# Kernel tuning notes

Hardware: AMD Instinct MI355X
Metric: run time of the kernel (lower is better)

## Reference

```python
import jax, jax.numpy as jnp
import numpy as np


def _rotate_half(x):
    x1, x2 = jnp.split(x, 2, axis=-1)
    return jnp.concatenate((-x2, x1), axis=-1)


def setup_inputs() -> dict:
    key = jax.random.key(0)
    ks = jax.random.split(key, 8)
    B, T, C, H = 2, 2048, 1024, 16
    Dh = C // H
    x = jax.random.normal(ks[0], (B, T, C), dtype=jnp.float32)
    # RoPE tables (T, head_dim)
    inv_freq = 1.0 / (10000.0 ** (np.arange(0, Dh, 2, dtype=np.float32) / Dh))
    pos = np.arange(T, dtype=np.float32)
    freqs = np.einsum('t,f->tf', pos, inv_freq)
    emb = np.concatenate([freqs, freqs], axis=-1)
    cos = jnp.asarray(np.cos(emb), dtype=jnp.float32)
    sin = jnp.asarray(np.sin(emb), dtype=jnp.float32)
    # causal mask: 1 where attending allowed, 0 elsewhere
    mask = jnp.tril(jnp.ones((T, T), dtype=jnp.int32))
    s = 0.02
    Wq = jax.random.normal(ks[1], (C, C), dtype=jnp.float32) * s
    Wk = jax.random.normal(ks[2], (C, C), dtype=jnp.float32) * s
    Wv = jax.random.normal(ks[3], (C, C), dtype=jnp.float32) * s
    Wo = jax.random.normal(ks[4], (C, C), dtype=jnp.float32) * s
    return {"x": x, "cos": cos, "sin": sin, "mask": mask, "n_heads": H,
            "Wq": Wq, "Wk": Wk, "Wv": Wv, "Wo": Wo}


def reference(x, cos, sin, mask, n_heads, Wq, Wk, Wv, Wo):
    B, T, C = x.shape
    H = n_heads
    Dh = C // H
    scale = Dh ** (-0.5)
    # projections (torch Linear: x @ W.T), reshape to (B, H, T, Dh)
    def proj(W):
        return (x @ W.T).reshape(B, T, H, Dh).transpose(0, 2, 1, 3)
    q, k, v = proj(Wq), proj(Wk), proj(Wv)
    # RoPE: cos/sin broadcast as (1, 1, T, Dh)
    c = cos[None, None]
    s = sin[None, None]
    q = q * c + _rotate_half(q) * s
    k = k * c + _rotate_half(k) * s
    att = jnp.einsum('bhtd,bhsd->bhts', q, k) * scale
    att = jnp.where(mask == 0, -jnp.inf, att)
    att = jax.nn.softmax(att, axis=-1)
    out = jnp.einsum('bhts,bhsd->bhtd', att, v)
    out = out.transpose(0, 2, 1, 3).reshape(B, T, C)
    return out @ Wo.T
```

## Files before the change

kernel.cpp:

```cpp
#include <hip/hip_runtime.h>
#include <stdint.h>

#define B_   2
#define T_   2048
#define C_   1024
#define H_   16
#define BT   4096
#define KDIM 1024

typedef unsigned short u16;
typedef __attribute__((ext_vector_type(8))) __bf16 bf16v8;
typedef __attribute__((ext_vector_type(4))) float f32x4;
typedef __attribute__((ext_vector_type(16))) float f32x16;
typedef __attribute__((ext_vector_type(4))) unsigned int u32x4;
typedef __attribute__((ext_vector_type(2))) unsigned int u32x2;

#define MFMA16(a, b, c) __builtin_amdgcn_mfma_f32_16x16x32_bf16((a), (b), (c), 0, 0, 0)
#define MFMA32(a, b, c) __builtin_amdgcn_mfma_f32_32x32x16_bf16((a), (b), (c), 0, 0, 0)

#define BARRIER() do { asm volatile("" ::: "memory"); \
                       __builtin_amdgcn_s_barrier();  \
                       asm volatile("" ::: "memory"); } while (0)

__device__ __forceinline__ u16 f2bf(float f) {
  __bf16 h = (__bf16)f;
  union { __bf16 h; u16 u; } v; v.h = h;
  return v.u;
}

__device__ __forceinline__ void xhalf(uint32_t a, uint32_t b,
                                      uint32_t& lo, uint32_t& hi) {
#if defined(__has_builtin) && __has_builtin(__builtin_amdgcn_permlane32_swap)
  u32x2 r = __builtin_amdgcn_permlane32_swap(a, b, false, false);
  lo = r.x; hi = r.y;
#else
  const bool upper = (threadIdx.x & 32) != 0;
  lo = upper ? __shfl_xor(b, 32) : a;
  hi = upper ? b : __shfl_xor(a, 32);
#endif
}

__device__ __forceinline__ void gload16(const void* g, void* l) {
  __builtin_amdgcn_global_load_lds((__attribute__((address_space(1))) void*)g,
                                   (__attribute__((address_space(3))) void*)l,
                                   16, 0, 0);
}

__global__ __launch_bounds__(256) void cvt_f32_bf16(const float* __restrict__ in,
                                                    u16* __restrict__ out, int n) {
  int i = (blockIdx.x * 256 + threadIdx.x) * 4;
  if (i + 3 < n) {
    float4 v = *(const float4*)(in + i);
    ushort4 o;
    o.x = f2bf(v.x); o.y = f2bf(v.y); o.z = f2bf(v.z); o.w = f2bf(v.w);
    *(ushort4*)(out + i) = o;
  }
}

__global__ __launch_bounds__(256) void cvt_weights(
    const float* __restrict__ wq, const float* __restrict__ wk,
    const float* __restrict__ wv, const float* __restrict__ wo,
    u16* __restrict__ qkv_dst, u16* __restrict__ o_dst) {
  const int bid = blockIdx.x;
  const int sel = bid >> 10;
  const float* src = (sel == 0) ? wq : (sel == 1) ? wk : (sel == 2) ? wv : wo;
  u16* dst = (sel < 3) ? (qkv_dst + sel * 1048576) : o_dst;
  const int i = ((bid & 1023) * 256 + threadIdx.x) * 4;
  float4 v = *(const float4*)(src + i);
  ushort4 o;
  o.x = f2bf(v.x); o.y = f2bf(v.y); o.z = f2bf(v.z); o.w = f2bf(v.w);
  *(ushort4*)(dst + i) = o;
}

template<int EPI, int NN>
__global__ __launch_bounds__(256, 2) void gemm128(
    const u16* __restrict__ A, const u16* __restrict__ Bm,
    float* __restrict__ Cf,
    u16* __restrict__ qo, u16* __restrict__ ko, u16* __restrict__ vt,
    const float* __restrict__ cosT, const float* __restrict__ sinT)
{
  __shared__ __align__(16) u16 As[2][128 * 64];
  __shared__ __align__(16) u16 Bs[2][128 * 64];
  const int tid = threadIdx.x;
  const int lane = tid & 63;
  const int w = tid >> 6;
  const int wm = w >> 1, wn = w & 1;
  const int lmod = lane & 15, ldiv = lane >> 4;

  constexpr int NBX = NN / 128;
  constexpr int XG_BY = (NBX == 24) ? 8 : 4;
  constexpr int XG_BX = (NBX == 24) ? 12 : 8;
  const int x = blockIdx.x & 7;
  const int i = blockIdx.x >> 3;
  const int gy = (NBX == 24) ? (x >> 1) : x;
  const int gx = (NBX == 24) ? (x & 1) : 0;
  const int by = gy * XG_BY + (i % XG_BY);
  const int bx = gx * XG_BX + (i / XG_BY);
  const int row0 = by * 128, col0 = bx * 128;

  const int srow = tid >> 3;
  const int sswz = ((tid & 7) * 16) ^ ((srow & 7) << 4);
  const char* Abase = (const char*)A + (size_t)(row0 + srow) * (KDIM * 2) + sswz;
  const char* Bbase = (const char*)Bm + (size_t)(col0 + srow) * (KDIM * 2) + sswz;
  const int ldst = (tid & 192) * 16;

  auto stage = [&](int buf, int t) {
    const int kb = t * 128;
#pragma unroll
    for (int c = 0; c < 4; ++c)
      gload16(Abase + (size_t)c * 32 * (KDIM * 2) + kb,
              (char*)As[buf] + c * 4096 + ldst);
#pragma unroll
    for (int c = 0; c < 4; ++c)
      gload16(Bbase + (size_t)c * 32 * (KDIM * 2) + kb,
              (char*)Bs[buf] + c * 4096 + ldst);
  };

  f32x4 acc[4][4] = {};
  stage(0, 0);

  for (int t = 0; t < KDIM / 64; ++t) {
    const int cur = t & 1;
    BARRIER();
    if (t + 1 < KDIM / 64) {
      stage(cur ^ 1, t + 1);
      asm volatile("s_waitcnt vmcnt(8)" ::: "memory");
    } else {
      asm volatile("s_waitcnt vmcnt(0)" ::: "memory");
    }
    BARRIER();

    bf16v8 af[4][2], bfr[4][2];
#pragma unroll
    for (int mf = 0; mf < 4; ++mf) {
      const int rr = wm * 64 + mf * 16 + lmod;
#pragma unroll
      for (int kc = 0; kc < 2; ++kc)
        af[mf][kc] = *(const bf16v8*)((const char*)As[cur] + rr * 128 +
                          ((kc * 64 + ldiv * 16) ^ ((rr & 7) << 4)));
    }
#pragma unroll
    for (int nf = 0; nf < 4; ++nf) {
      const int rr = wn * 64 + nf * 16 + lmod;
#pragma unroll
      for (int kc = 0; kc < 2; ++kc)
        bfr[nf][kc] = *(const bf16v8*)((const char*)Bs[cur] + rr * 128 +
                          ((kc * 64 + ldiv * 16) ^ ((rr & 7) << 4)));
    }
#pragma unroll
    for (int kc = 0; kc < 2; ++kc)
#pragma unroll
      for (int mf = 0; mf < 4; ++mf)
#pragma unroll
        for (int nf = 0; nf < 4; ++nf)
          acc[mf][nf] = MFMA16(af[mf][kc], bfr[nf][kc], acc[mf][nf]);
  }

  if (EPI == 0) {
#pragma unroll
    for (int mf = 0; mf < 4; ++mf) {
      const int mbase = row0 + wm * 64 + mf * 16 + ldiv * 4;
#pragma unroll
      for (int nf = 0; nf < 4; ++nf) {
        const int n = col0 + wn * 64 + nf * 16 + lmod;
#pragma unroll
        for (int r = 0; r < 4; ++r)
          Cf[(size_t)(mbase + r) * NN + n] = acc[mf][nf][r];
      }
    }
  } else {
    const int nb = col0 + wn * 64;
    const int proj = nb >> 10;
    const int hh = (nb & 1023) >> 6;
    if (proj < 2) {
      u16* dst = proj ? ko : qo;
#pragma unroll
      for (int mf = 0; mf < 4; ++mf) {
#pragma unroll
        for (int r = 0; r < 4; ++r) {
          const int m = row0 + wm * 64 + mf * 16 + ldiv * 4 + r;
          const int b = m >> 11, t = m & 2047;
          u16* drow = dst + ((size_t)(b * H_ + hh) * T_ + t) * 64;
#pragma unroll
          for (int nf = 0; nf < 4; ++nf) {
            const int d = nf * 16 + lmod;
            const float cs = cosT[t * 64 + d];
            const float sn = sinT[t * 64 + d];
            const float other = (nf < 2) ? acc[mf][nf + 2][r] : acc[mf][nf - 2][r];
            float val = (nf < 2) ? (acc[mf][nf][r] * cs - other * sn)
                                 : (acc[mf][nf][r] * cs + other * sn);
            if (proj == 0) val *= 0.18033688011112042f;
            drow[d] = f2bf(val);
          }
        }
      }
    } else {
      BARRIER();
      char* scr = (char*)As + w * 8192;
#pragma unroll
      for (int nf = 0; nf < 4; ++nf)
#pragma unroll
        for (int mf = 0; mf < 4; ++mf)
#pragma unroll
          for (int rp = 0; rp < 2; ++rp) {
            const int dd = nf * 16 + lmod;
            const int t0 = mf * 16 + ldiv * 4 + rp * 2;
            const uint32_t pk = (uint32_t)f2bf(acc[mf][nf][rp * 2]) |
                                ((uint32_t)f2bf(acc[mf][nf][rp * 2 + 1]) << 16);
            *(uint32_t*)(scr + ((dd * 128 + t0 * 2) ^ ((dd & 7) << 4))) = pk;
          }
      __syncthreads();
      const int trow = row0 + wm * 64;
      const int bb = trow >> 11, tl = trow & 2047;
#pragma unroll
      for (int j = 0; j < 8; ++j) {
        const int dd = j * 8 + (lane >> 3);
        const int c = lane & 7;
        const u32x4 vv = *(const u32x4*)(scr + ((dd * 128 + c * 16) ^ ((dd & 7) << 4)));
        u16* drow = vt + ((size_t)((bb * H_ + hh) * 64 + dd)) * T_ + tl;
        *(u32x4*)((char*)drow + c * 16) = vv;
      }
    }
  }
}

__global__ __launch_bounds__(256, 2) void attn_fwd3(
    const u16* __restrict__ Q, const u16* __restrict__ K,
    const u16* __restrict__ Vt, u16* __restrict__ O)
{
  __shared__ __align__(16) u16 Kl[2][64 * 64];
  __shared__ __align__(16) u16 Vl[2][64 * 64];
  const int xcd = blockIdx.x & 7;
  const int idx = blockIdx.x >> 3;
  const int h   = idx & 1;
  const int j   = idx >> 1;
  const int bh  = xcd * 4 + (j & 3);
  const int cr  = j >> 2;
  const int chunk = h ? (15 - cr) : cr;
  const int qb0 = chunk * 128;
  const int nblk = 2 * chunk + 2;

  const int tid = threadIdx.x, lane = tid & 63, w = tid >> 6;
  const int l31 = lane & 31, hi = lane >> 5;
  const int qrow = qb0 + w * 32;

  bf16v8 qf[4];
  {
    const u16* qp = Q + ((size_t)bh * T_ + qrow + l31) * 64 + hi * 8;
    qf[0] = *(const bf16v8*)(qp);
    qf[1] = *(const bf16v8*)(qp + 16);
    qf[2] = *(const bf16v8*)(qp + 32);
    qf[3] = *(const bf16v8*)(qp + 48);
  }

  float m2 = -1e30f, lsum = 0.f;
  f32x16 oacc0 = {}, oacc1 = {};

  const int scolb = (tid & 7) * 16;
  const int ldst = (tid & 192) * 16;

  auto stage = [&](int buf, int t) {
    const int s0 = t << 6;
#pragma unroll
    for (int c = 0; c < 2; ++c) {
      const int row = (c * 256 + tid) >> 3;
      const int sw = scolb ^ ((row & 7) << 4);
      gload16((const char*)(K + ((size_t)bh * T_ + s0 + row) * 64) + sw,
              (char*)Kl[buf] + c * 4096 + ldst);
    }
#pragma unroll
    for (int c = 0; c < 2; ++c) {
      const int row = (c * 256 + tid) >> 3;
      const int sw = scolb ^ ((row & 7) << 4);
      gload16((const char*)(Vt + ((size_t)(bh * 64 + row)) * T_ + s0) + sw,
              (char*)Vl[buf] + c * 4096 + ldst);
    }
  };

  auto substep = [&](int cur, int sub, int s0_sub) {
    bf16v8 kf[4], vf[4];
#pragma unroll
    for (int c = 0; c < 4; ++c) {
      const int row = sub * 32 + l31;
      kf[c] = *(const bf16v8*)((const char*)Kl[cur] + row * 128 +
                  ((c * 32 + hi * 16) ^ ((row & 7) << 4)));
    }
#pragma unroll
    for (int db = 0; db < 2; ++db)
#pragma unroll
      for (int kg = 0; kg < 2; ++kg) {
        const int row = db * 32 + l31;
        vf[db * 2 + kg] = *(const bf16v8*)((const char*)Vl[cur] + row * 128 +
                  ((sub * 64 + kg * 32 + hi * 16) ^ ((row & 7) << 4)));
      }
    f32x16 s = {};
    s = MFMA32(kf[0], qf[0], s);
    s = MFMA32(kf[1], qf[1], s);
    s = MFMA32(kf[2], qf[2], s);
    s = MFMA32(kf[3], qf[3], s);
    if (s0_sub + 31 > qrow) {
#pragma unroll
      for (int r = 0; r < 16; ++r) {
        const int key = s0_sub + (r & 3) + 8 * (r >> 2) + 4 * hi;
        if (key > qrow + l31) s[r] = -1e30f;
      }
    }
    float t8[8];
#pragma unroll
    for (int r = 0; r < 8; ++r) t8[r] = fmaxf(s[r], s[r + 8]);
    float t4a = fmaxf(t8[0], t8[4]), t4b = fmaxf(t8[1], t8[5]);
    float t4c = fmaxf(t8[2], t8[6]), t4d = fmaxf(t8[3], t8[7]);
    float pmax = fmaxf(fmaxf(t4a, t4b), fmaxf(t4c, t4d));
    {
      uint32_t lo, hh2;
      xhalf(__builtin_bit_cast(uint32_t, pmax), __builtin_bit_cast(uint32_t, pmax), lo, hh2);
      pmax = fmaxf(__builtin_bit_cast(float, lo), __builtin_bit_cast(float, hh2));
    }
    if (!__all(pmax <= m2 + 11.5416f)) {
      const float mnew = fmaxf(m2, pmax);
      const float rs = __builtin_amdgcn_exp2f(m2 - mnew);
      lsum *= rs;
#pragma unroll
      for (int r = 0; r < 16; ++r) { oacc0[r] *= rs; oacc1[r] *= rs; }
      m2 = mnew;
    }
    float p[16];
#pragma unroll
    for (int r = 0; r < 16; ++r) p[r] = __builtin_amdgcn_exp2f(s[r] - m2);
    float a8[8];
#pragma unroll
    for (int r = 0; r < 8; ++r) a8[r] = p[r] + p[r + 8];
    float a4a = a8[0] + a8[4], a4b = a8[1] + a8[5];
    float a4c = a8[2] + a8[6], a4d = a8[3] + a8[7];
    float ts = (a4a + a4b) + (a4c + a4d);
    {
      uint32_t lo, hh2;
      xhalf(__builtin_bit_cast(uint32_t, ts), __builtin_bit_cast(uint32_t, ts), lo, hh2);
      ts = __builtin_bit_cast(float, lo) + __builtin_bit_cast(float, hh2);
    }
    lsum += ts;
    uint32_t o[8];
#pragma unroll
    for (int jj = 0; jj < 8; ++jj) {
      const int r0 = 4 * (jj >> 1) + 2 * (jj & 1);
      uint32_t d;
      asm("v_cvt_pk_bf16_f32 %0, %1, %2" : "=v"(d) : "v"(p[r0]), "v"(p[r0 + 1]));
      o[jj] = d;
    }
#pragma unroll
    for (int kg = 0; kg < 2; ++kg) {
      uint32_t f0, f1, f2, f3;
      xhalf(o[4 * kg + 0], o[4 * kg + 2], f0, f2);
      xhalf(o[4 * kg + 1], o[4 * kg + 3], f1, f3);
      u32x4 fr;
      fr.x = f0; fr.y = f1; fr.z = f2; fr.w = f3;
      const bf16v8 pf = __builtin_bit_cast(bf16v8, fr);
      oacc0 = MFMA32(vf[kg], pf, oacc0);
      oacc1 = MFMA32(vf[2 + kg], pf, oacc1);
    }
  };

  stage(0, 0);
  for (int t = 0; t < nblk; ++t) {
    const int cur = t & 1;
    BARRIER();
    if (t + 1 < nblk) {
      stage(cur ^ 1, t + 1);
      asm volatile("s_waitcnt vmcnt(8)" ::: "memory");
    } else {
      asm volatile("s_waitcnt vmcnt(0)" ::: "memory");
    }
    BARRIER();
#pragma unroll
    for (int sub = 0; sub < 2; ++sub) {
      const int s0_sub = t * 64 + sub * 32;
      if (s0_sub <= qrow + 31) substep(cur, sub, s0_sub);
    }
  }

  BARRIER();
  char* scr = (char*)Kl + w * 4096;
  const float inv = 1.f / lsum;
#pragma unroll
  for (int r2 = 0; r2 < 8; ++r2) {
    const int r = r2 * 2;
    const int dd = (r & 3) + 8 * (r >> 2) + 4 * hi;
    const uint32_t pk0 = (uint32_t)f2bf(oacc0[r] * inv) |
                         ((uint32_t)f2bf(oacc0[r + 1] * inv) << 16);
    *(uint32_t*)(scr + ((l31 * 128 + dd * 2) ^ ((l31 & 7) << 4))) = pk0;
    const uint32_t pk1 = (uint32_t)f2bf(oacc1[r] * inv) |
                         ((uint32_t)f2bf(oacc1[r + 1] * inv) << 16);
    *(uint32_t*)(scr + ((l31 * 128 + (dd + 32) * 2) ^ ((l31 & 7) << 4))) = pk1;
  }
  __syncthreads();
  const int b = bh >> 4, hh = bh & 15;
  const int qq = lane >> 1, cc = lane & 1;
  u16* orow = O + ((size_t)(b * T_ + qrow + qq)) * C_ + hh * 64 + cc * 32;
#pragma unroll
  for (int jj = 0; jj < 4; ++jj) {
    const u32x4 vv = *(const u32x4*)(scr + ((qq * 128 + cc * 64 + jj * 16) ^ ((qq & 7) << 4)));
    *(u32x4*)((char*)orow + jj * 16) = vv;
  }
}

extern "C" void kernel_launch(void* const* d_in, const int* in_sizes, int n_in,
                              void* d_out, int out_size, void* d_ws, size_t ws_size,
                              hipStream_t stream) {
  const float* x    = (const float*)d_in[0];
  const float* cosT = (const float*)d_in[1];
  const float* sinT = (const float*)d_in[2];
  const float* Wq = (const float*)d_in[5];
  const float* Wk = (const float*)d_in[6];
  const float* Wv = (const float*)d_in[7];
  const float* Wo = (const float*)d_in[8];
  float* out = (float*)d_out;

  char* ws = (char*)d_ws;
  u16* xb   = (u16*)(ws);
  u16* wqkv = (u16*)(ws + 8388608);
  u16* wo   = (u16*)(ws + 14680064);
  u16* q    = (u16*)(ws + 16777216);
  u16* k    = (u16*)(ws + 25165824);
  u16* vt   = (u16*)(ws + 33554432);
  u16* aout = (u16*)(ws + 41943040);

  cvt_f32_bf16<<<4096, 256, 0, stream>>>(x, xb, BT * C_);
  cvt_weights<<<4096, 256, 0, stream>>>(Wq, Wk, Wv, Wo, wqkv, wo);

  gemm128<1, 3072><<<768, 256, 0, stream>>>(xb, wqkv, nullptr,
                                            q, k, vt, cosT, sinT);
  attn_fwd3<<<512, 256, 0, stream>>>(q, k, vt, aout);
  gemm128<0, 1024><<<256, 256, 0, stream>>>(aout, wo, out,
                                            nullptr, nullptr, nullptr,
                                            nullptr, nullptr);
}
```

Measured before the change: 118.4 us.

## Split long causal query chunks across two blocks and merge with a combine kernel

The attention kernel now gives the eight short query chunks to one block each and splits each of the eight long chunks' key ranges into two halves handled by separate blocks. This raises the grid from 512 to 768 blocks and roughly halves the longest per-block key loop. Split blocks write unnormalised bf16 partial outputs plus per-row max and sum into reused workspace. A new combine kernel rescales and merges the two halves into the final output. The cost is an extra kernel launch, extra global traffic for the partials, and bf16 rounding of the unnormalised partials.

```diff
diff --git a/kernel.cpp b/kernel.cpp
--- a/kernel.cpp
+++ b/kernel.cpp
@@ -26,6 +26,10 @@
   __bf16 h = (__bf16)f;
   union { __bf16 h; u16 u; } v; v.h = h;
   return v.u;
+}
+__device__ __forceinline__ float bf2f(u16 u) {
+  union { uint32_t u; float f; } v; v.u = (uint32_t)u << 16;
+  return v.f;
 }
 
 __device__ __forceinline__ void xhalf(uint32_t a, uint32_t b,
@@ -224,21 +228,28 @@
   }
 }
 
-__global__ __launch_bounds__(256, 2) void attn_fwd3(
+__global__ __launch_bounds__(256, 2) void attn_fwd4(
     const u16* __restrict__ Q, const u16* __restrict__ K,
-    const u16* __restrict__ Vt, u16* __restrict__ O)
+    const u16* __restrict__ Vt, u16* __restrict__ O,
+    u16* __restrict__ part_o, float* __restrict__ pml)
 {
   __shared__ __align__(16) u16 Kl[2][64 * 64];
   __shared__ __align__(16) u16 Vl[2][64 * 64];
   const int xcd = blockIdx.x & 7;
-  const int idx = blockIdx.x >> 3;
-  const int h   = idx & 1;
-  const int j   = idx >> 1;
-  const int bh  = xcd * 4 + (j & 3);
-  const int cr  = j >> 2;
-  const int chunk = h ? (15 - cr) : cr;
-  const int qb0 = chunk * 128;
-  const int nblk = 2 * chunk + 2;
+  const int i   = blockIdx.x >> 3;
+  const int bh  = xcd * 4 + (i & 3);
+  const int r   = i >> 2;
+  int qb0, t0, t1, sid;
+  if (r < 8) {
+    qb0 = r * 128; t0 = 0; t1 = 2 * r + 2; sid = -1;
+  } else {
+    const int s = r - 8;
+    const int c = 8 + (s >> 1);
+    const int half = s & 1;
+    qb0 = c * 128;
+    t0 = half * (c + 1); t1 = t0 + (c + 1);
+    sid = (bh * 8 + (c - 8)) * 2 + half;
+  }
 
   const int tid = threadIdx.x, lane = tid & 63, w = tid >> 6;
   const int l31 = lane & 31, hi = lane >> 5;
@@ -300,14 +311,14 @@
     s = MFMA32(kf[3], qf[3], s);
     if (s0_sub + 31 > qrow) {
 #pragma unroll
-      for (int r = 0; r < 16; ++r) {
-        const int key = s0_sub + (r & 3) + 8 * (r >> 2) + 4 * hi;
-        if (key > qrow + l31) s[r] = -1e30f;
+      for (int r2 = 0; r2 < 16; ++r2) {
+        const int key = s0_sub + (r2 & 3) + 8 * (r2 >> 2) + 4 * hi;
+        if (key > qrow + l31) s[r2] = -1e30f;
       }
     }
     float t8[8];
 #pragma unroll
-    for (int r = 0; r < 8; ++r) t8[r] = fmaxf(s[r], s[r + 8]);
+    for (int r2 = 0; r2 < 8; ++r2) t8[r2] = fmaxf(s[r2], s[r2 + 8]);
     float t4a = fmaxf(t8[0], t8[4]), t4b = fmaxf(t8[1], t8[5]);
     float t4c = fmaxf(t8[2], t8[6]), t4d = fmaxf(t8[3], t8[7]);
     float pmax = fmaxf(fmaxf(t4a, t4b), fmaxf(t4c, t4d));
@@ -321,15 +332,15 @@
       const float rs = __builtin_amdgcn_exp2f(m2 - mnew);
       lsum *= rs;
 #pragma unroll
-      for (int r = 0; r < 16; ++r) { oacc0[r] *= rs; oacc1[r] *= rs; }
+      for (int r2 = 0; r2 < 16; ++r2) { oacc0[r2] *= rs; oacc1[r2] *= rs; }
       m2 = mnew;
     }
     float p[16];
 #pragma unroll
-    for (int r = 0; r < 16; ++r) p[r] = __builtin_amdgcn_exp2f(s[r] - m2);
+    for (int r2 = 0; r2 < 16; ++r2) p[r2] = __builtin_amdgcn_exp2f(s[r2] - m2);
     float a8[8];
 #pragma unroll
-    for (int r = 0; r < 8; ++r) a8[r] = p[r] + p[r + 8];
+    for (int r2 = 0; r2 < 8; ++r2) a8[r2] = p[r2] + p[r2 + 8];
     float a4a = a8[0] + a8[4], a4b = a8[1] + a8[5];
     float a4c = a8[2] + a8[6], a4d = a8[3] + a8[7];
     float ts = (a4a + a4b) + (a4c + a4d);
@@ -360,11 +371,11 @@
     }
   };
 
-  stage(0, 0);
-  for (int t = 0; t < nblk; ++t) {
-    const int cur = t & 1;
+  stage(0, t0);
+  for (int t = t0; t < t1; ++t) {
+    const int cur = (t - t0) & 1;
     BARRIER();
-    if (t + 1 < nblk) {
+    if (t + 1 < t1) {
       stage(cur ^ 1, t + 1);
       asm volatile("s_waitcnt vmcnt(8)" ::: "memory");
     } else {
@@ -380,7 +391,7 @@
 
   BARRIER();
   char* scr = (char*)Kl + w * 4096;
-  const float inv = 1.f / lsum;
+  const float inv = (sid < 0) ? (1.f / lsum) : 1.f;
 #pragma unroll
   for (int r2 = 0; r2 < 8; ++r2) {
     const int r = r2 * 2;
@@ -393,13 +404,61 @@
     *(uint32_t*)(scr + ((l31 * 128 + (dd + 32) * 2) ^ ((l31 & 7) << 4))) = pk1;
   }
   __syncthreads();
+  const int qq = lane >> 1, cc = lane & 1;
+  if (sid < 0) {
+    const int b = bh >> 4, hh = bh & 15;
+    u16* orow = O + ((size_t)(b * T_ + qrow + qq)) * C_ + hh * 64 + cc * 32;
+#pragma unroll
+    for (int jj = 0; jj < 4; ++jj) {
+      const u32x4 vv = *(const u32x4*)(scr + ((qq * 128 + cc * 64 + jj * 16) ^ ((qq & 7) << 4)));
+      *(u32x4*)((char*)orow + jj * 16) = vv;
+    }
+  } else {
+    u16* prow = part_o + ((size_t)(sid * 128 + w * 32 + qq)) * 64 + cc * 32;
+#pragma unroll
+    for (int jj = 0; jj < 4; ++jj) {
+      const u32x4 vv = *(const u32x4*)(scr + ((qq * 128 + cc * 64 + jj * 16) ^ ((qq & 7) << 4)));
+      *(u32x4*)((char*)prow + jj * 16) = vv;
+    }
+    if (lane < 32) {
+      pml[sid * 256 + w * 32 + lane] = m2;
+      pml[sid * 256 + 128 + w * 32 + lane] = lsum;
+    }
+  }
+}
+
+__global__ __launch_bounds__(256) void attn_combine(
+    const u16* __restrict__ part_o, const float* __restrict__ pml,
+    u16* __restrict__ O)
+{
+  const int combo = blockIdx.x;
+  const int bh = combo >> 3, c8 = combo & 7;
+  const int sid0 = (bh * 8 + c8) * 2;
+  const int row = threadIdx.x >> 1, dh = threadIdx.x & 1;
+  const float m0 = pml[sid0 * 256 + row];
+  const float l0 = pml[sid0 * 256 + 128 + row];
+  const float m1 = pml[(sid0 + 1) * 256 + row];
+  const float l1 = pml[(sid0 + 1) * 256 + 128 + row];
+  const float m = fmaxf(m0, m1);
+  const float s0 = __builtin_amdgcn_exp2f(m0 - m);
+  const float s1 = __builtin_amdgcn_exp2f(m1 - m);
+  const float inv = 1.f / (l0 * s0 + l1 * s1);
+  const u16* p0 = part_o + ((size_t)(sid0 * 128 + row)) * 64 + dh * 32;
+  const u16* p1 = part_o + ((size_t)((sid0 + 1) * 128 + row)) * 64 + dh * 32;
   const int b = bh >> 4, hh = bh & 15;
-  const int qq = lane >> 1, cc = lane & 1;
-  u16* orow = O + ((size_t)(b * T_ + qrow + qq)) * C_ + hh * 64 + cc * 32;
-#pragma unroll
-  for (int jj = 0; jj < 4; ++jj) {
-    const u32x4 vv = *(const u32x4*)(scr + ((qq * 128 + cc * 64 + jj * 16) ^ ((qq & 7) << 4)));
-    *(u32x4*)((char*)orow + jj * 16) = vv;
+  const int t = (8 + c8) * 128 + row;
+  u16* dst = O + ((size_t)(b * T_ + t)) * C_ + hh * 64 + dh * 32;
+#pragma unroll
+  for (int j0 = 0; j0 < 4; ++j0) {
+    const u32x4 a = *(const u32x4*)(p0 + j0 * 8);
+    const u32x4 bq = *(const u32x4*)(p1 + j0 * 8);
+    const u16* pa = (const u16*)&a;
+    const u16* pb = (const u16*)&bq;
+    u16 outv[8];
+#pragma unroll
+    for (int j = 0; j < 8; ++j)
+      outv[j] = f2bf((bf2f(pa[j]) * s0 + bf2f(pb[j]) * s1) * inv);
+    *(u32x4*)(dst + j0 * 8) = *(const u32x4*)outv;
   }
 }
 
@@ -423,13 +482,16 @@
   u16* k    = (u16*)(ws + 25165824);
   u16* vt   = (u16*)(ws + 33554432);
   u16* aout = (u16*)(ws + 41943040);
+  u16* part_o = xb;
+  float* pml  = (float*)(ws + 8388608);
 
   cvt_f32_bf16<<<4096, 256, 0, stream>>>(x, xb, BT * C_);
   cvt_weights<<<4096, 256, 0, stream>>>(Wq, Wk, Wv, Wo, wqkv, wo);
 
   gemm128<1, 3072><<<768, 256, 0, stream>>>(xb, wqkv, nullptr,
                                             q, k, vt, cosT, sinT);
-  attn_fwd3<<<512, 256, 0, stream>>>(q, k, vt, aout);
+  attn_fwd4<<<768, 256, 0, stream>>>(q, k, vt, aout, part_o, pml);
+  attn_combine<<<256, 256, 0, stream>>>(part_o, pml, aout);
   gemm128<0, 1024><<<256, 256, 0, stream>>>(aout, wo, out,
                                             nullptr, nullptr, nullptr,
                                             nullptr, nullptr);
```

After: 116.1 us. 2.0% less time.
